# Kernel tuning notes

Hardware: AMD Instinct MI355X
Metric: run time of the kernel (lower is better)

## Reference

```python
import jax, jax.numpy as jnp
import numpy as np
from functools import partial

NSEG = 1024  # N+1: superpixel ids in [0, NSEG)


def setup_inputs() -> dict:
    key = jax.random.key(0)
    k1, k2, k3, k4 = jax.random.split(key, 4)
    pred = jax.random.normal(k1, (4, 21, 512, 512), dtype=jnp.float32)
    Laplace_W = jax.random.normal(k2, (4, NSEG, NSEG), dtype=jnp.float32)
    Laplace_L = jax.random.normal(k3, (4, NSEG, NSEG), dtype=jnp.float32)
    image_spiex = jax.random.randint(k4, (4, 512, 512), 0, NSEG, dtype=jnp.int64)
    return {"pred": pred, "Laplace_W": Laplace_W, "Laplace_L": Laplace_L,
            "image_spiex": image_spiex}


def reference(pred, Laplace_W, Laplace_L, image_spiex):
    b, C, x, y = pred.shape  # C = 21 classes
    nseg = Laplace_L.shape[1]  # N + 1
    ids = image_spiex.reshape(b, -1)  # [b, x*y]
    # Original sums the masked [count, 21] block over BOTH dims, then divides
    # by pixel count -> a scalar per superpixel broadcast to all 21 channels.
    px_sum = pred.sum(axis=1).reshape(b, -1)  # [b, x*y] sum over channels
    seg = partial(jax.ops.segment_sum, num_segments=nseg)
    seg_sum = jax.vmap(seg)(px_sum, ids)                           # [b, nseg]
    counts = jax.vmap(seg)(jnp.ones_like(px_sum), ids)             # [b, nseg]
    m = jnp.where(counts > 0, seg_sum / jnp.where(counts > 0, counts, 1.0), 0.0)
    # result[k] has 21 identical columns = m, so
    # trace(result^T @ L @ result) = 21 * m^T L m
    quad = jnp.einsum('bn,bnm,bm->b', m, Laplace_L, m)
    w_norm = jnp.sqrt(jnp.sum(Laplace_W * Laplace_W, axis=(1, 2)))  # Frobenius
    loss = (2.0 / w_norm) * (C * quad)
    return loss.sum()
```

## Files before the change

### kernel.cpp

```cpp
#include <hip/hip_runtime.h>
#include <hip/hip_bf16.h>

#define NSEG 1024
#define PIX (512 * 512)
#define NCH 21

#define OFF_PSUM 0
#define OFF_PCNT (64 * 4 * 1024)
#define OFF_M    (2 * 64 * 4 * 1024)
#define OFF_CTRL (OFF_M + 4 * 1024)
#define C_QUAD(b) (32 * (b))
#define C_WSS(b)  (128 + 32 * (b))
#define C_BCNT(b) (256 + 32 * (b))
#define C_GDONE   (384)

#define QBLK 64
#define WBLK 16
#define XBLK (QBLK + WBLK)

__device__ __forceinline__ void bf16x2_to_f32(unsigned u, float& a, float& b) {
    a = __uint_as_float(u << 16);
    b = __uint_as_float(u & 0xffff0000u);
}

__device__ __forceinline__ int f32_sig_u32(unsigned w) {
    const unsigned e0 = (w >> 7) & 0xFFu, e1 = (w >> 23) & 0xFFu;
    return (int)(((e0 > 0u && e0 < 64u) || e0 >= 192u) ||
                 ((e1 > 0u && e1 < 64u) || e1 >= 192u));
}

__global__ __launch_bounds__(512) void seg_kernel(const void* __restrict__ pred_,
                                                  const void* __restrict__ ids_,
                                                  float* __restrict__ part_sum,
                                                  float* __restrict__ part_cnt) {
    __shared__ float s_sum[NSEG];
    __shared__ float s_cnt[NSEG];
    __shared__ int s_flags[2];
    const int b = blockIdx.y;
    const int t = threadIdx.x;

    if (t < 64) {
        const uint2 pv = reinterpret_cast<const uint2*>(pred_)[t];
        const uint2 iv = reinterpret_cast<const uint2*>(ids_)[t];
        const int pf = __any(f32_sig_u32(pv.x) | f32_sig_u32(pv.y));
        const int i64 = !__any((int)(iv.y != 0u));
        if (t == 0) { s_flags[0] = pf; s_flags[1] = i64; }
    }
    for (int i = t; i < NSEG; i += 512) { s_sum[i] = 0.f; s_cnt[i] = 0.f; }
    __syncthreads();
    const int f32p = s_flags[0];
    const int i64  = s_flags[1];

    const int base = blockIdx.x * 4096 + t * 8;
    const size_t poff = (size_t)b * NCH * PIX + base;

    float acc[8];
#pragma unroll
    for (int i = 0; i < 8; ++i) acc[i] = 0.f;

    if (f32p) {
        const float* predb = (const float*)pred_ + poff;
#pragma unroll
        for (int c = 0; c < NCH; ++c) {
            const float4 v0 = *reinterpret_cast<const float4*>(predb + (size_t)c * PIX);
            const float4 v1 = *reinterpret_cast<const float4*>(predb + (size_t)c * PIX + 4);
            acc[0] += v0.x; acc[1] += v0.y; acc[2] += v0.z; acc[3] += v0.w;
            acc[4] += v1.x; acc[5] += v1.y; acc[6] += v1.z; acc[7] += v1.w;
        }
    } else {
        const __hip_bfloat16* predb = (const __hip_bfloat16*)pred_ + poff;
#pragma unroll
        for (int c = 0; c < NCH; ++c) {
            const uint4 v = *reinterpret_cast<const uint4*>(predb + (size_t)c * PIX);
            float a, bb;
            bf16x2_to_f32(v.x, a, bb); acc[0] += a; acc[1] += bb;
            bf16x2_to_f32(v.y, a, bb); acc[2] += a; acc[3] += bb;
            bf16x2_to_f32(v.z, a, bb); acc[4] += a; acc[5] += bb;
            bf16x2_to_f32(v.w, a, bb); acc[6] += a; acc[7] += bb;
        }
    }

    int id[8];
    if (i64) {
        const int4* iv = reinterpret_cast<const int4*>((const long long*)ids_ + (size_t)b * PIX + base);
        const int4 q0 = iv[0], q1 = iv[1], q2 = iv[2], q3 = iv[3];
        id[0] = q0.x; id[1] = q0.z; id[2] = q1.x; id[3] = q1.z;
        id[4] = q2.x; id[5] = q2.z; id[6] = q3.x; id[7] = q3.z;
    } else {
        const int4* iv = reinterpret_cast<const int4*>((const int*)ids_ + (size_t)b * PIX + base);
        const int4 q0 = iv[0], q1 = iv[1];
        id[0] = q0.x; id[1] = q0.y; id[2] = q0.z; id[3] = q0.w;
        id[4] = q1.x; id[5] = q1.y; id[6] = q1.z; id[7] = q1.w;
    }

#pragma unroll
    for (int i = 0; i < 8; ++i) {
        const int s = id[i] & (NSEG - 1);
        atomicAdd(&s_sum[s], acc[i]);
        atomicAdd(&s_cnt[s], 1.f);
    }

    __syncthreads();
    float* ps = part_sum + ((size_t)b * 64 + blockIdx.x) * NSEG;
    float* pc = part_cnt + ((size_t)b * 64 + blockIdx.x) * NSEG;
    for (int i = t; i < NSEG; i += 512) { ps[i] = s_sum[i]; pc[i] = s_cnt[i]; }
}

__global__ __launch_bounds__(128) void mbuild_kernel(const float* __restrict__ part_sum,
                                                     const float* __restrict__ part_cnt,
                                                     float* __restrict__ m,
                                                     float* __restrict__ ctrl) {
    const int b = blockIdx.y;
    const int col = blockIdx.x * 128 + threadIdx.x;
    float s = 0.f, c = 0.f;
    const float* ps = part_sum + (size_t)b * 64 * NSEG + col;
    const float* pc = part_cnt + (size_t)b * 64 * NSEG + col;
#pragma unroll 8
    for (int p = 0; p < 64; ++p) {
        s += ps[(size_t)p * NSEG];
        c += pc[(size_t)p * NSEG];
    }
    m[b * NSEG + col] = c > 0.f ? s / c : 0.f;
    if (blockIdx.x == 0 && b == 0) {
        for (int i = threadIdx.x; i < 512; i += 128) ctrl[i] = 0.f;
    }
}

__global__ __launch_bounds__(256) void quad_kernel(const void* __restrict__ L_,
                                                   const void* __restrict__ W_,
                                                   const float* __restrict__ m,
                                                   float* __restrict__ ctrl,
                                                   float* __restrict__ out) {
    __shared__ int s_f32;
    __shared__ float s_part[4];
    const int b = blockIdx.y;
    const int t = threadIdx.x;
    const int lane = t & 63;
    const int wave = t >> 6;
    const bool is_quad = blockIdx.x < QBLK;

    if (t < 64) {
        const uint2 v = reinterpret_cast<const uint2*>(is_quad ? L_ : W_)[t];
        const int f = __any(f32_sig_u32(v.x) | f32_sig_u32(v.y));
        if (t == 0) s_f32 = f;
    }
    __syncthreads();
    const int f32x = s_f32;

    float acc = 0.f;
    if (is_quad) {
        const float* mb = m + b * NSEG;
        const float2* m2 = reinterpret_cast<const float2*>(mb);
        float mreg[16];
#pragma unroll
        for (int j = 0; j < 8; ++j) {
            const float2 mv = m2[lane + 64 * j];
            mreg[2 * j] = mv.x; mreg[2 * j + 1] = mv.y;
        }
        const int row0 = blockIdx.x * 16 + wave * 4;
#pragma unroll
        for (int r = 0; r < 4; ++r) {
            const int n = row0 + r;
            const float mn = mb[n];
            float d = 0.f;
            if (f32x) {
                const float2* row = reinterpret_cast<const float2*>((const float*)L_ + (size_t)b * NSEG * NSEG + (size_t)n * NSEG);
#pragma unroll
                for (int j = 0; j < 8; ++j) {
                    const float2 p = row[lane + 64 * j];
                    d += p.x * mreg[2 * j] + p.y * mreg[2 * j + 1];
                }
            } else {
                const unsigned* row = reinterpret_cast<const unsigned*>((const __hip_bfloat16*)L_ + (size_t)b * NSEG * NSEG + (size_t)n * NSEG);
#pragma unroll
                for (int j = 0; j < 8; ++j) {
                    float a, bb;
                    bf16x2_to_f32(row[lane + 64 * j], a, bb);
                    d += a * mreg[2 * j] + bb * mreg[2 * j + 1];
                }
            }
            acc += mn * d;
        }
    } else {
        const int k = blockIdx.x - QBLK;
        if (f32x) {
            const float4* Wv = reinterpret_cast<const float4*>((const float*)W_ + (size_t)b * NSEG * NSEG + (size_t)k * 65536);
            for (int it = t; it < 16384; it += 256) {
                const float4 v = Wv[it];
                acc += v.x * v.x + v.y * v.y + v.z * v.z + v.w * v.w;
            }
        } else {
            const uint4* Wv = reinterpret_cast<const uint4*>((const __hip_bfloat16*)W_ + (size_t)b * NSEG * NSEG + (size_t)k * 65536);
            for (int it = t; it < 8192; it += 256) {
                const uint4 v = Wv[it];
                float a, bb;
                bf16x2_to_f32(v.x, a, bb); acc += a * a + bb * bb;
                bf16x2_to_f32(v.y, a, bb); acc += a * a + bb * bb;
                bf16x2_to_f32(v.z, a, bb); acc += a * a + bb * bb;
                bf16x2_to_f32(v.w, a, bb); acc += a * a + bb * bb;
            }
        }
    }

#pragma unroll
    for (int off = 32; off; off >>= 1) acc += __shfl_down(acc, off);
    if (lane == 0) s_part[wave] = acc;
    __syncthreads();
    if (t == 0) {
        const float blocksum = s_part[0] + s_part[1] + s_part[2] + s_part[3];
        atomicAdd(&ctrl[is_quad ? C_QUAD(b) : C_WSS(b)], blocksum);
        __threadfence();
        if (atomicAdd((int*)&ctrl[C_BCNT(b)], 1) == XBLK - 1) {
            if (atomicAdd((int*)&ctrl[C_GDONE], 1) == 3) {
                float loss = 0.f;
#pragma unroll
                for (int i = 0; i < 4; ++i) {
                    const float q = atomicAdd(&ctrl[C_QUAD(i)], 0.f);
                    const float w = atomicAdd(&ctrl[C_WSS(i)], 0.f);
                    loss += (2.0f / sqrtf(w)) * 21.0f * q;
                }
                out[0] = loss;
            }
        }
    }
}

extern "C" void kernel_launch(void* const* d_in, const int* in_sizes, int n_in,
                              void* d_out, int out_size, void* d_ws, size_t ws_size,
                              hipStream_t stream) {
    const void* pred = d_in[0];
    const void* W    = d_in[1];
    const void* L    = d_in[2];
    const void* ids  = d_in[3];

    float* ws       = (float*)d_ws;
    float* part_sum = ws + OFF_PSUM;
    float* part_cnt = ws + OFF_PCNT;
    float* m        = ws + OFF_M;
    float* ctrl     = ws + OFF_CTRL;

    seg_kernel<<<dim3(64, 4), 512, 0, stream>>>(pred, ids, part_sum, part_cnt);
    mbuild_kernel<<<dim3(8, 4), 128, 0, stream>>>(part_sum, part_cnt, m, ctrl);
    quad_kernel<<<dim3(XBLK, 4), 256, 0, stream>>>(L, W, m, ctrl, (float*)d_out);
}
```

Measured before the change: 216.0 us.

## Split quad and W-norm work one row per wave; finalize in separate kernel

The quadratic-form and Frobenius-norm kernel now assigns one matrix row per wave across 512 blocks per batch, instead of 80 blocks doing 16 rows or 64K elements each. This gives more blocks to spread the L and W streaming reads across the GPU. Each row uses vectorized float4/uint4 loads. The global atomic accumulation and last-block-done counter scheme is replaced by per-block partial writes plus a small final reduction kernel. That removes atomics and counter resets but adds one more kernel launch.

```diff
diff --git a/kernel.cpp b/kernel.cpp
--- a/kernel.cpp
+++ b/kernel.cpp
@@ -5,18 +5,11 @@
 #define PIX (512 * 512)
 #define NCH 21
 
-#define OFF_PSUM 0
-#define OFF_PCNT (64 * 4 * 1024)
-#define OFF_M    (2 * 64 * 4 * 1024)
-#define OFF_CTRL (OFF_M + 4 * 1024)
-#define C_QUAD(b) (32 * (b))
-#define C_WSS(b)  (128 + 32 * (b))
-#define C_BCNT(b) (256 + 32 * (b))
-#define C_GDONE   (384)
-
-#define QBLK 64
-#define WBLK 16
-#define XBLK (QBLK + WBLK)
+#define OFF_PSUM  0
+#define OFF_PCNT  (64 * 4 * 1024)
+#define OFF_M     (2 * 64 * 4 * 1024)
+#define OFF_QPART (OFF_M + 4 * 1024)
+#define OFF_WPART (OFF_QPART + 4 * 256)
 
 __device__ __forceinline__ void bf16x2_to_f32(unsigned u, float& a, float& b) {
     a = __uint_as_float(u << 16);
@@ -108,8 +101,7 @@
 
 __global__ __launch_bounds__(128) void mbuild_kernel(const float* __restrict__ part_sum,
                                                      const float* __restrict__ part_cnt,
-                                                     float* __restrict__ m,
-                                                     float* __restrict__ ctrl) {
+                                                     float* __restrict__ m) {
     const int b = blockIdx.y;
     const int col = blockIdx.x * 128 + threadIdx.x;
     float s = 0.f, c = 0.f;
@@ -121,23 +113,20 @@
         c += pc[(size_t)p * NSEG];
     }
     m[b * NSEG + col] = c > 0.f ? s / c : 0.f;
-    if (blockIdx.x == 0 && b == 0) {
-        for (int i = threadIdx.x; i < 512; i += 128) ctrl[i] = 0.f;
-    }
 }
 
 __global__ __launch_bounds__(256) void quad_kernel(const void* __restrict__ L_,
                                                    const void* __restrict__ W_,
                                                    const float* __restrict__ m,
-                                                   float* __restrict__ ctrl,
-                                                   float* __restrict__ out) {
+                                                   float* __restrict__ qpart,
+                                                   float* __restrict__ wpart) {
     __shared__ int s_f32;
     __shared__ float s_part[4];
     const int b = blockIdx.y;
     const int t = threadIdx.x;
     const int lane = t & 63;
     const int wave = t >> 6;
-    const bool is_quad = blockIdx.x < QBLK;
+    const bool is_quad = blockIdx.x < 256;
 
     if (t < 64) {
         const uint2 v = reinterpret_cast<const uint2*>(is_quad ? L_ : W_)[t];
@@ -147,52 +136,53 @@
     __syncthreads();
     const int f32x = s_f32;
 
-    float acc = 0.f;
+    float res = 0.f;
     if (is_quad) {
+        const int n = blockIdx.x * 4 + wave;
         const float* mb = m + b * NSEG;
-        const float2* m2 = reinterpret_cast<const float2*>(mb);
-        float mreg[16];
-#pragma unroll
-        for (int j = 0; j < 8; ++j) {
-            const float2 mv = m2[lane + 64 * j];
-            mreg[2 * j] = mv.x; mreg[2 * j + 1] = mv.y;
-        }
-        const int row0 = blockIdx.x * 16 + wave * 4;
-#pragma unroll
-        for (int r = 0; r < 4; ++r) {
-            const int n = row0 + r;
-            const float mn = mb[n];
-            float d = 0.f;
-            if (f32x) {
-                const float2* row = reinterpret_cast<const float2*>((const float*)L_ + (size_t)b * NSEG * NSEG + (size_t)n * NSEG);
-#pragma unroll
-                for (int j = 0; j < 8; ++j) {
-                    const float2 p = row[lane + 64 * j];
-                    d += p.x * mreg[2 * j] + p.y * mreg[2 * j + 1];
-                }
-            } else {
-                const unsigned* row = reinterpret_cast<const unsigned*>((const __hip_bfloat16*)L_ + (size_t)b * NSEG * NSEG + (size_t)n * NSEG);
-#pragma unroll
-                for (int j = 0; j < 8; ++j) {
-                    float a, bb;
-                    bf16x2_to_f32(row[lane + 64 * j], a, bb);
-                    d += a * mreg[2 * j] + bb * mreg[2 * j + 1];
-                }
-            }
-            acc += mn * d;
-        }
+        const float4* m4 = reinterpret_cast<const float4*>(mb);
+        float d = 0.f;
+        if (f32x) {
+            const float4* row = reinterpret_cast<const float4*>((const float*)L_ + (size_t)b * NSEG * NSEG + (size_t)n * NSEG);
+#pragma unroll
+            for (int j = 0; j < 4; ++j) {
+                const float4 rv = row[lane + 64 * j];
+                const float4 mv = m4[lane + 64 * j];
+                d += rv.x * mv.x + rv.y * mv.y + rv.z * mv.z + rv.w * mv.w;
+            }
+        } else {
+            const uint4* row = reinterpret_cast<const uint4*>((const __hip_bfloat16*)L_ + (size_t)b * NSEG * NSEG + (size_t)n * NSEG);
+#pragma unroll
+            for (int j = 0; j < 2; ++j) {
+                const uint4 rv = row[lane + 64 * j];
+                const float4 m0 = m4[2 * (lane + 64 * j)];
+                const float4 m1 = m4[2 * (lane + 64 * j) + 1];
+                float a, bb;
+                bf16x2_to_f32(rv.x, a, bb); d += a * m0.x + bb * m0.y;
+                bf16x2_to_f32(rv.y, a, bb); d += a * m0.z + bb * m0.w;
+                bf16x2_to_f32(rv.z, a, bb); d += a * m1.x + bb * m1.y;
+                bf16x2_to_f32(rv.w, a, bb); d += a * m1.z + bb * m1.w;
+            }
+        }
+        res = d;
+#pragma unroll
+        for (int off = 32; off; off >>= 1) res += __shfl_down(res, off);
+        if (lane == 0) s_part[wave] = mb[n] * res;
     } else {
-        const int k = blockIdx.x - QBLK;
+        const int n = (blockIdx.x - 256) * 4 + wave;
+        float acc = 0.f;
         if (f32x) {
-            const float4* Wv = reinterpret_cast<const float4*>((const float*)W_ + (size_t)b * NSEG * NSEG + (size_t)k * 65536);
-            for (int it = t; it < 16384; it += 256) {
-                const float4 v = Wv[it];
+            const float4* row = reinterpret_cast<const float4*>((const float*)W_ + (size_t)b * NSEG * NSEG + (size_t)n * NSEG);
+#pragma unroll
+            for (int j = 0; j < 4; ++j) {
+                const float4 v = row[lane + 64 * j];
                 acc += v.x * v.x + v.y * v.y + v.z * v.z + v.w * v.w;
             }
         } else {
-            const uint4* Wv = reinterpret_cast<const uint4*>((const __hip_bfloat16*)W_ + (size_t)b * NSEG * NSEG + (size_t)k * 65536);
-            for (int it = t; it < 8192; it += 256) {
-                const uint4 v = Wv[it];
+            const uint4* row = reinterpret_cast<const uint4*>((const __hip_bfloat16*)W_ + (size_t)b * NSEG * NSEG + (size_t)n * NSEG);
+#pragma unroll
+            for (int j = 0; j < 2; ++j) {
+                const uint4 v = row[lane + 64 * j];
                 float a, bb;
                 bf16x2_to_f32(v.x, a, bb); acc += a * a + bb * bb;
                 bf16x2_to_f32(v.y, a, bb); acc += a * a + bb * bb;
@@ -200,29 +190,40 @@
                 bf16x2_to_f32(v.w, a, bb); acc += a * a + bb * bb;
             }
         }
-    }
-
-#pragma unroll
-    for (int off = 32; off; off >>= 1) acc += __shfl_down(acc, off);
-    if (lane == 0) s_part[wave] = acc;
+#pragma unroll
+        for (int off = 32; off; off >>= 1) acc += __shfl_down(acc, off);
+        if (lane == 0) s_part[wave] = acc;
+    }
+
     __syncthreads();
     if (t == 0) {
         const float blocksum = s_part[0] + s_part[1] + s_part[2] + s_part[3];
-        atomicAdd(&ctrl[is_quad ? C_QUAD(b) : C_WSS(b)], blocksum);
-        __threadfence();
-        if (atomicAdd((int*)&ctrl[C_BCNT(b)], 1) == XBLK - 1) {
-            if (atomicAdd((int*)&ctrl[C_GDONE], 1) == 3) {
-                float loss = 0.f;
-#pragma unroll
-                for (int i = 0; i < 4; ++i) {
-                    const float q = atomicAdd(&ctrl[C_QUAD(i)], 0.f);
-                    const float w = atomicAdd(&ctrl[C_WSS(i)], 0.f);
-                    loss += (2.0f / sqrtf(w)) * 21.0f * q;
-                }
-                out[0] = loss;
-            }
-        }
-    }
+        if (is_quad) qpart[b * 256 + blockIdx.x] = blocksum;
+        else         wpart[b * 256 + (blockIdx.x - 256)] = blocksum;
+    }
+}
+
+__global__ __launch_bounds__(256) void final_kernel(const float* __restrict__ qpart,
+                                                    const float* __restrict__ wpart,
+                                                    float* __restrict__ out) {
+    __shared__ float sl[4];
+    const int t = threadIdx.x;
+    const int b = t >> 6;
+    const int lane = t & 63;
+    float q = 0.f, w = 0.f;
+#pragma unroll
+    for (int j = 0; j < 4; ++j) {
+        q += qpart[b * 256 + lane + 64 * j];
+        w += wpart[b * 256 + lane + 64 * j];
+    }
+#pragma unroll
+    for (int off = 32; off; off >>= 1) {
+        q += __shfl_down(q, off);
+        w += __shfl_down(w, off);
+    }
+    if (lane == 0) sl[b] = (2.0f / sqrtf(w)) * 21.0f * q;
+    __syncthreads();
+    if (t == 0) out[0] = sl[0] + sl[1] + sl[2] + sl[3];
 }
 
 extern "C" void kernel_launch(void* const* d_in, const int* in_sizes, int n_in,
@@ -237,9 +238,11 @@
     float* part_sum = ws + OFF_PSUM;
     float* part_cnt = ws + OFF_PCNT;
     float* m        = ws + OFF_M;
-    float* ctrl     = ws + OFF_CTRL;
+    float* qpart    = ws + OFF_QPART;
+    float* wpart    = ws + OFF_WPART;
 
     seg_kernel<<<dim3(64, 4), 512, 0, stream>>>(pred, ids, part_sum, part_cnt);
-    mbuild_kernel<<<dim3(8, 4), 128, 0, stream>>>(part_sum, part_cnt, m, ctrl);
-    quad_kernel<<<dim3(XBLK, 4), 256, 0, stream>>>(L, W, m, ctrl, (float*)d_out);
-}
+    mbuild_kernel<<<dim3(8, 4), 128, 0, stream>>>(part_sum, part_cnt, m);
+    quad_kernel<<<dim3(512, 4), 256, 0, stream>>>(L, W, m, qpart, wpart);
+    final_kernel<<<1, 256, 0, stream>>>(qpart, wpart, (float*)d_out);
+}
```

Result: faster. 178.6 us (-17.3%).
